# Kernel tuning notes

Hardware: AMD Instinct MI355X
Metric: run time of the kernel (lower is better)

Reference implementation:

```python
import jax, jax.numpy as jnp
import numpy as np

B = 32768
DNA, IMG, FUSED, HEADS = 768, 512, 256, 4
HEAD_DIM = FUSED // HEADS
GENUS, SPECIES, MAXSP = 372, 1050, 23
RED, GEMB, SDH, DEC_HID = 128, 64, 64, 744


def setup_inputs() -> dict:
    key = jax.random.key(0)
    ks = iter(jax.random.split(key, 40))
    p = lambda *shape: jax.random.normal(next(ks), shape, jnp.float32) * 0.02
    z = lambda n: jnp.zeros((n,), jnp.float32)
    inp = {
        'dna_emb': jax.random.normal(next(ks), (B, DNA), jnp.float32),
        'img_emb': jax.random.normal(next(ks), (B, IMG), jnp.float32),
        # AttentionFusion params
        'W_dna': p(DNA, FUSED), 'b_dna': z(FUSED),
        'W_img': p(IMG, FUSED), 'b_img': z(FUSED),
        'W_qkv': p(FUSED, 3 * FUSED), 'b_qkv': z(3 * FUSED),
        'W_o': p(FUSED, FUSED), 'b_o': z(FUSED),
        'W_f1': p(FUSED, FUSED), 'b_f1': z(FUSED),
        'W_f2': p(FUSED, FUSED), 'b_f2': z(FUSED),
        # genus Decoder params
        'W_d1': p(FUSED, DEC_HID), 'b_d1': z(DEC_HID),
        'W_d2': p(DEC_HID, GENUS), 'b_d2': z(GENUS),
        # SpeciePredictor params
        'W_fp': p(FUSED, RED), 'b_fp': z(RED),
        'W_ge': p(GENUS, GEMB), 'b_ge': z(GEMB),
        'W_s1': p(RED + GEMB, SDH), 'b_s1': z(SDH),
        'W_s2': p(SDH, MAXSP), 'b_s2': z(MAXSP),
        # precomputed scatter->gather indices: species s -> (genus s%372, local s//372)
        'species_genus': jnp.arange(SPECIES, dtype=jnp.int32) % GENUS,
        'species_local': jnp.arange(SPECIES, dtype=jnp.int32) // GENUS,
    }
    return inp


def _forward(dna_emb, img_emb, W_dna, b_dna, W_img, b_img, W_qkv, b_qkv, W_o, b_o,
             W_f1, b_f1, W_f2, b_f2, W_d1, b_d1, W_d2, b_d2, W_fp, b_fp,
             W_ge, b_ge, W_s1, b_s1, W_s2, b_s2, species_genus, species_local):
    # --- AttentionFusion ---
    dna_proj = dna_emb @ W_dna + b_dna                     # [B, F]
    img_proj = img_emb @ W_img + b_img                     # [B, F]
    seq = jnp.stack([dna_proj, img_proj], axis=1)          # [B, 2, F]
    qkv = seq @ W_qkv + b_qkv                              # [B, 2, 3F]
    q, k, v = jnp.split(qkv, 3, axis=-1)
    q = q.reshape(B, 2, HEADS, HEAD_DIM)
    k = k.reshape(B, 2, HEADS, HEAD_DIM)
    v = v.reshape(B, 2, HEADS, HEAD_DIM)
    scale = 1.0 / np.sqrt(HEAD_DIM).astype(np.float32)
    scores = jnp.einsum('bqhd,bkhd->bhqk', q, k) * scale   # [B, H, 2, 2]
    attn = jax.nn.softmax(scores, axis=-1)
    ctx = jnp.einsum('bhqk,bkhd->bqhd', attn, v).reshape(B, 2, FUSED)
    attn_out = ctx @ W_o + b_o                             # [B, 2, F]
    fused = attn_out.mean(axis=1)                          # [B, F]
    fused = jax.nn.relu(fused @ W_f1 + b_f1) @ W_f2 + b_f2
    # --- genus Decoder (Linear -> Sigmoid -> Linear -> softmax) ---
    genus_logits = jax.nn.softmax(
        jax.nn.sigmoid(fused @ W_d1 + b_d1) @ W_d2 + b_d2, axis=1)  # [B, 372]
    # --- species head ---
    reduced_fused = fused @ W_fp + b_fp                    # [B, 128]
    genus_emb = genus_logits @ W_ge + b_ge                 # [B, 64]
    genus_fused = jnp.concatenate([genus_emb, reduced_fused], axis=1)  # [B, 192]
    local_logits = jax.nn.sigmoid(genus_fused @ W_s1 + b_s1) @ W_s2 + b_s2  # [B, 23]
    # --- _flatten_species_probs_batch, fused: result[:, s] = genus_logits[:, g(s)] * local_logits[:, l(s)]
    # (avoids materializing the [B, 372, 23] outer product)
    species_probs = genus_logits[:, species_genus] * local_logits[:, species_local]  # [B, 1050]
    return species_probs, local_logits, genus_logits, fused, reduced_fused


def reference(dna_emb, img_emb, W_dna, b_dna, W_img, b_img, W_qkv, b_qkv, W_o, b_o,
              W_f1, b_f1, W_f2, b_f2, W_d1, b_d1, W_d2, b_d2, W_fp, b_fp,
              W_ge, b_ge, W_s1, b_s1, W_s2, b_s2, species_genus, species_local):
    return _forward(dna_emb, img_emb, W_dna, b_dna, W_img, b_img, W_qkv, b_qkv,
                    W_o, b_o, W_f1, b_f1, W_f2, b_f2, W_d1, b_d1, W_d2, b_d2,
                    W_fp, b_fp, W_ge, b_ge, W_s1, b_s1, W_s2, b_s2,
                    species_genus, species_local)
```

## Files before the change

kernel.cpp:

```cpp
#include <hip/hip_runtime.h>
#include <hip/hip_bf16.h>

typedef __hip_bfloat16 bf16;
typedef __attribute__((ext_vector_type(8))) short short8_t;
typedef __attribute__((ext_vector_type(4))) float f32x4;

#define B_ROWS 32768

__device__ __forceinline__ float to_f(float x) { return x; }
__device__ __forceinline__ float to_f(bf16 x) { return __bfloat162float(x); }

__device__ __forceinline__ unsigned short f2bf(float f) {
    union { float f; unsigned int u; } c; c.f = f;
    unsigned int u = c.u;
    unsigned int rb = ((u >> 16) & 1u) + 0x7fffu;
    return (unsigned short)((u + rb) >> 16);
}

__device__ __forceinline__ void stage8(const bf16* __restrict__ src, bf16* dst) {
    *(uint4*)dst = *(const uint4*)src;
}
__device__ __forceinline__ void stage8(const float* __restrict__ src, bf16* dst) {
    const float4 a = *(const float4*)src;
    const float4 b = *(const float4*)(src + 4);
    union { uint4 u; unsigned short h[8]; } r;
    r.h[0] = f2bf(a.x); r.h[1] = f2bf(a.y); r.h[2] = f2bf(a.z); r.h[3] = f2bf(a.w);
    r.h[4] = f2bf(b.x); r.h[5] = f2bf(b.y); r.h[6] = f2bf(b.z); r.h[7] = f2bf(b.w);
    *(uint4*)dst = r.u;
}

template <typename TA, int ACT>
__global__ __launch_bounds__(256) void gemm_mfma(
    const TA* __restrict__ A, int lda,
    const bf16* __restrict__ Wt, int kpad,
    const float* __restrict__ bias,
    float* __restrict__ outf, int ldof,
    bf16* __restrict__ outb, int ldob,
    int M, int N, int nstore, int K)
{
    __shared__ __align__(16) bf16 As[128 * 64];
    __shared__ __align__(16) bf16 Bs[128 * 64];

    const int tid = threadIdx.x;
    const int lane = tid & 63;
    const int w = tid >> 6;
    const int wr = w >> 1, wc = w & 1;
    const int m0 = blockIdx.y * 128, n0 = blockIdx.x * 128;
    const int kq = lane >> 4, lr = lane & 15;

    f32x4 acc[4][4] = {};

    const int srow = tid >> 3;
    const int sch = tid & 7;
    const int sx = sch ^ (srow & 7);

    for (int k0 = 0; k0 < K; k0 += 64) {
#pragma unroll
        for (int p = 0; p < 4; ++p) {
            const int row = srow + p * 32;
            const int dst = row * 64 + (sx << 3);
            stage8(A + (size_t)(m0 + row) * lda + (k0 + sch * 8), &As[dst]);
            stage8(Wt + (size_t)(n0 + row) * kpad + (k0 + sch * 8), &Bs[dst]);
        }
        __syncthreads();
#pragma unroll
        for (int kk = 0; kk < 2; ++kk) {
            const int co = ((kk * 4 + kq) ^ (lr & 7)) << 3;
            short8_t am[4], wf[4];
#pragma unroll
            for (int i = 0; i < 4; ++i) {
                am[i] = *(const short8_t*)&As[(wr * 64 + i * 16 + lr) * 64 + co];
                wf[i] = *(const short8_t*)&Bs[(wc * 64 + i * 16 + lr) * 64 + co];
            }
#pragma unroll
            for (int i = 0; i < 4; ++i)
#pragma unroll
                for (int j = 0; j < 4; ++j)
                    acc[i][j] = __builtin_amdgcn_mfma_f32_16x16x32_bf16(
                        wf[j], am[i], acc[i][j], 0, 0, 0);
        }
        __syncthreads();
    }

#pragma unroll
    for (int mi = 0; mi < 4; ++mi) {
        const size_t m = m0 + wr * 64 + mi * 16 + lr;
#pragma unroll
        for (int ni = 0; ni < 4; ++ni) {
            const int nb = n0 + wc * 64 + ni * 16 + 4 * kq;
            if (nb >= nstore) continue;
            float vv[4];
#pragma unroll
            for (int r = 0; r < 4; ++r) {
                const int n = nb + r;
                float v = acc[mi][ni][r] + ((n < N) ? bias[n] : 0.f);
                if (ACT == 1) v = fmaxf(v, 0.f);
                if (ACT == 2) v = (n < N) ? 1.f / (1.f + __expf(-v)) : 0.f;
                vv[r] = v;
            }
            if (outf) {
                if (nb + 3 < N) {
                    float4 f4; f4.x = vv[0]; f4.y = vv[1]; f4.z = vv[2]; f4.w = vv[3];
                    *(float4*)&outf[m * ldof + nb] = f4;
                } else {
#pragma unroll
                    for (int r = 0; r < 4; ++r)
                        if (nb + r < N) outf[m * ldof + nb + r] = vv[r];
                }
            }
            if (outb) {
                if (nb + 3 < nstore) {
                    union { uint2 u; unsigned short h[4]; } pk;
                    pk.h[0] = f2bf(vv[0]); pk.h[1] = f2bf(vv[1]);
                    pk.h[2] = f2bf(vv[2]); pk.h[3] = f2bf(vv[3]);
                    *(uint2*)&outb[m * ldob + nb] = pk.u;
                } else {
#pragma unroll
                    for (int r = 0; r < 4; ++r)
                        if (nb + r < nstore)
                            ((unsigned short*)outb)[m * ldob + nb + r] = f2bf(vv[r]);
                }
            }
        }
    }
}

struct PrepackArgs {
    const float* src[12];
    unsigned long long off[12];
    int K[12], N[12], Kpad[12], Nr[12];
};

__global__ __launch_bounds__(256) void prepack_kernel(PrepackArgs a, bf16* wsbase)
{
    const int wI = blockIdx.y;
    const float* __restrict__ src = a.src[wI];
    bf16* dst = wsbase + a.off[wI];
    const int K = a.K[wI], N = a.N[wI], Kpad = a.Kpad[wI];
    const int total = a.Nr[wI] * Kpad;
    for (int e = blockIdx.x * 256 + threadIdx.x; e < total; e += gridDim.x * 256) {
        const int n = e / Kpad, k = e - n * Kpad;
        const float v = (n < N && k < K) ? src[(size_t)k * N + n] : 0.f;
        ((unsigned short*)dst)[e] = f2bf(v);
    }
}

__global__ __launch_bounds__(256) void attn_kernel(
    const bf16* __restrict__ qkv, bf16* __restrict__ ctxm)
{
    const int b = blockIdx.x;
    const int lane = threadIdx.x & 63;
    const bf16* base = qkv + (size_t)b * 1536;
    const int o = (threadIdx.x >> 6) * 64 + lane;

    float q0 = to_f(base[o]),       k0 = to_f(base[256 + o]),       v0 = to_f(base[512 + o]);
    float q1 = to_f(base[768 + o]), k1 = to_f(base[768 + 256 + o]), v1 = to_f(base[768 + 512 + o]);

    float s00 = q0 * k0, s01 = q0 * k1, s10 = q1 * k0, s11 = q1 * k1;
#pragma unroll
    for (int off = 32; off; off >>= 1) {
        s00 += __shfl_xor(s00, off);
        s01 += __shfl_xor(s01, off);
        s10 += __shfl_xor(s10, off);
        s11 += __shfl_xor(s11, off);
    }
    const float sc = 0.125f;
    s00 *= sc; s01 *= sc; s10 *= sc; s11 *= sc;

    float m0 = fmaxf(s00, s01);
    float e00 = __expf(s00 - m0), e01 = __expf(s01 - m0);
    float r0 = 1.f / (e00 + e01);
    float m1 = fmaxf(s10, s11);
    float e10 = __expf(s10 - m1), e11 = __expf(s11 - m1);
    float r1 = 1.f / (e10 + e11);

    float c0 = e00 * r0 * v0 + e01 * r0 * v1;
    float c1 = e10 * r1 * v0 + e11 * r1 * v1;
    ctxm[(size_t)b * 256 + o] = __float2bfloat16(0.5f * (c0 + c1));
}

__global__ __launch_bounds__(64) void softmax372_kernel(
    const bf16* __restrict__ in, float* __restrict__ outf, bf16* __restrict__ outb)
{
    const int b = blockIdx.x;
    const int lane = threadIdx.x;
    const bf16* row = in + (size_t)b * 372;

    float v[6];
    float mx = -1e30f;
#pragma unroll
    for (int i = 0; i < 6; ++i) {
        int idx = lane + i * 64;
        v[i] = (idx < 372) ? to_f(row[idx]) : -1e30f;
        mx = fmaxf(mx, v[i]);
    }
#pragma unroll
    for (int off = 32; off; off >>= 1) mx = fmaxf(mx, __shfl_xor(mx, off));

    float s = 0.f;
#pragma unroll
    for (int i = 0; i < 6; ++i) {
        int idx = lane + i * 64;
        if (idx < 372) { v[i] = __expf(v[i] - mx); s += v[i]; }
    }
#pragma unroll
    for (int off = 32; off; off >>= 1) s += __shfl_xor(s, off);
    float r = 1.f / s;

#pragma unroll
    for (int i = 0; i < 6; ++i) {
        int idx = lane + i * 64;
        if (idx < 372) {
            float p = v[i] * r;
            outf[(size_t)b * 372 + idx] = p;
            outb[(size_t)b * 384 + idx] = __float2bfloat16(p);
        } else if (idx < 384) {
            outb[(size_t)b * 384 + idx] = __float2bfloat16(0.f);
        }
    }
}

__global__ __launch_bounds__(256) void species_kernel(
    const float* __restrict__ g, const float* __restrict__ ll,
    const int* __restrict__ sg, const int* __restrict__ sl,
    float* __restrict__ out)
{
    const int s = blockIdx.x * 256 + threadIdx.x;
    const int b = blockIdx.y;
    if (s < 1050) {
        out[(size_t)b * 1050 + s] =
            g[(size_t)b * 372 + sg[s]] * ll[(size_t)b * 23 + sl[s]];
    }
}

extern "C" void kernel_launch(void* const* d_in, const int* in_sizes, int n_in,
                              void* d_out, int out_size, void* d_ws, size_t ws_size,
                              hipStream_t stream)
{
    const int B = B_ROWS;
    const float* dna   = (const float*)d_in[0];
    const float* img   = (const float*)d_in[1];
    const float* W_dna = (const float*)d_in[2];  const float* b_dna = (const float*)d_in[3];
    const float* W_img = (const float*)d_in[4];  const float* b_img = (const float*)d_in[5];
    const float* W_qkv = (const float*)d_in[6];  const float* b_qkv = (const float*)d_in[7];
    const float* W_o   = (const float*)d_in[8];  const float* b_o   = (const float*)d_in[9];
    const float* W_f1  = (const float*)d_in[10]; const float* b_f1  = (const float*)d_in[11];
    const float* W_f2  = (const float*)d_in[12]; const float* b_f2  = (const float*)d_in[13];
    const float* W_d1  = (const float*)d_in[14]; const float* b_d1  = (const float*)d_in[15];
    const float* W_d2  = (const float*)d_in[16]; const float* b_d2  = (const float*)d_in[17];
    const float* W_fp  = (const float*)d_in[18]; const float* b_fp  = (const float*)d_in[19];
    const float* W_ge  = (const float*)d_in[20]; const float* b_ge  = (const float*)d_in[21];
    const float* W_s1  = (const float*)d_in[22]; const float* b_s1  = (const float*)d_in[23];
    const float* W_s2  = (const float*)d_in[24]; const float* b_s2  = (const float*)d_in[25];
    const int*   sg    = (const int*)d_in[26];
    const int*   sl    = (const int*)d_in[27];

    bf16* ws = (bf16*)d_ws;

    static const int KK[12] = {768, 512, 256, 256, 256, 256, 256, 744, 256, 372, 192, 64};
    static const int NN[12] = {256, 256, 768, 256, 256, 256, 744, 372, 128,  64,  64, 23};
    const float* SRC[12] = {W_dna, W_img, W_qkv, W_o, W_f1, W_f2, W_d1, W_d2, W_fp, W_ge, W_s1, W_s2};
    PrepackArgs pa;
    size_t woff[12];
    size_t off = 0;
    for (int i = 0; i < 12; ++i) {
        pa.src[i] = SRC[i]; pa.K[i] = KK[i]; pa.N[i] = NN[i];
        pa.Kpad[i] = (KK[i] + 63) & ~63;
        pa.Nr[i]   = (NN[i] + 127) & ~127;
        pa.off[i] = off; woff[i] = off;
        off += (size_t)pa.Kpad[i] * pa.Nr[i];
    }
    const size_t AOFF = off;

    bf16* seq  = ws + AOFF;
    bf16* qkvc = ws + AOFF + (size_t)B * 512;
    bf16* ctxm = ws + AOFF + (size_t)B * 896;
    bf16* t1   = ws + AOFF;
    bf16* t2   = ws + AOFF + (size_t)B * 256;
    bf16* fbuf = ws + AOFF;
    bf16* h1   = ws + AOFF + (size_t)B * 256;
    bf16* g    = ws + AOFF + (size_t)B * 1024;
    bf16* gbf  = ws + AOFF + (size_t)B * 256;
    bf16* gf   = ws + AOFF + (size_t)B * 640;
    bf16* sh   = ws + AOFF + (size_t)B * 832;

    float* out       = (float*)d_out;
    float* o_species = out;
    float* o_local   = out + (size_t)B * 1050;
    float* o_genus   = out + (size_t)B * 1073;
    float* o_fused   = out + (size_t)B * 1445;
    float* o_red     = out + (size_t)B * 1701;

    prepack_kernel<<<dim3(32, 12), 256, 0, stream>>>(pa, ws);

#define NOF (float*)nullptr, 0
#define NOB (bf16*)nullptr, 0

    gemm_mfma<float, 0><<<dim3(2, 256), 256, 0, stream>>>(
        dna, 768, ws + woff[0], 768, b_dna, NOF, seq, 512, B, 256, 256, 768);
    gemm_mfma<float, 0><<<dim3(2, 256), 256, 0, stream>>>(
        img, 512, ws + woff[1], 512, b_img, NOF, seq + 256, 512, B, 256, 256, 512);
    for (int c = 0; c < 4; ++c) {
        gemm_mfma<bf16, 0><<<dim3(6, 128), 256, 0, stream>>>(
            seq + (size_t)c * (B / 2) * 256, 256, ws + woff[2], 256, b_qkv,
            NOF, qkvc, 768, B / 2, 768, 768, 256);
        attn_kernel<<<B / 4, 256, 0, stream>>>(qkvc, ctxm + (size_t)c * (B / 4) * 256);
    }
    gemm_mfma<bf16, 0><<<dim3(2, 256), 256, 0, stream>>>(
        ctxm, 256, ws + woff[3], 256, b_o, NOF, t1, 256, B, 256, 256, 256);
    gemm_mfma<bf16, 1><<<dim3(2, 256), 256, 0, stream>>>(
        t1, 256, ws + woff[4], 256, b_f1, NOF, t2, 256, B, 256, 256, 256);
    gemm_mfma<bf16, 0><<<dim3(2, 256), 256, 0, stream>>>(
        t2, 256, ws + woff[5], 256, b_f2, o_fused, 256, fbuf, 256, B, 256, 256, 256);
    gemm_mfma<bf16, 2><<<dim3(6, 256), 256, 0, stream>>>(
        fbuf, 256, ws + woff[6], 256, b_d1, NOF, h1, 768, B, 744, 768, 256);
    gemm_mfma<bf16, 0><<<dim3(3, 256), 256, 0, stream>>>(
        h1, 768, ws + woff[7], 768, b_d2, NOF, g, 372, B, 372, 372, 768);
    softmax372_kernel<<<B, 64, 0, stream>>>(g, o_genus, gbf);
    gemm_mfma<bf16, 0><<<dim3(1, 256), 256, 0, stream>>>(
        gbf, 384, ws + woff[9], 384, b_ge, NOF, gf, 192, B, 64, 64, 384);
    gemm_mfma<bf16, 0><<<dim3(1, 256), 256, 0, stream>>>(
        fbuf, 256, ws + woff[8], 256, b_fp, o_red, 128, gf + 64, 192, B, 128, 128, 256);
    gemm_mfma<bf16, 2><<<dim3(1, 256), 256, 0, stream>>>(
        gf, 192, ws + woff[10], 192, b_s1, NOF, sh, 64, B, 64, 64, 192);
    gemm_mfma<bf16, 0><<<dim3(1, 256), 256, 0, stream>>>(
        sh, 64, ws + woff[11], 64, b_s2, o_local, 23, NOB, B, 23, 23, 64);
    species_kernel<<<dim3(5, B), 256, 0, stream>>>(o_genus, o_local, sg, sl, o_species);
#undef NOF
#undef NOB
}
```

Before: 854.8 us.

## Fuse fusion MLP chain, use direct-to-LDS loads, widen GEMM tiles, unchunk QKV

Several changes land together. A new mlp3 kernel chains the W_o, W_f1 and W_f2 GEMMs per 128-row tile, keeping the intermediates in shared memory instead of writing them to global memory. GEMM staging of bf16 data now goes through global_load_lds straight into LDS, and most GEMMs use a 256-wide N tile with 512 threads. The QKV GEMM and attention run once over the whole batch instead of in four chunks, and the weight prepack uses a shared-memory transpose. This cuts global memory traffic and launch count, at the cost of much more LDS per block (the mlp3 kernel uses about 112KB), which may limit occupancy.

```diff
diff --git a/kernel.cpp b/kernel.cpp
--- a/kernel.cpp
+++ b/kernel.cpp
@@ -17,10 +17,13 @@
     return (unsigned short)((u + rb) >> 16);
 }
 
-__device__ __forceinline__ void stage8(const bf16* __restrict__ src, bf16* dst) {
-    *(uint4*)dst = *(const uint4*)src;
-}
-__device__ __forceinline__ void stage8(const float* __restrict__ src, bf16* dst) {
+__device__ __forceinline__ void glds16(const void* g, void* s) {
+    __builtin_amdgcn_global_load_lds(
+        (const __attribute__((address_space(1))) unsigned int*)g,
+        (__attribute__((address_space(3))) unsigned int*)s, 16, 0, 0);
+}
+
+__device__ __forceinline__ void stage8f(const float* __restrict__ src, bf16* dst) {
     const float4 a = *(const float4*)src;
     const float4 b = *(const float4*)(src + 4);
     union { uint4 u; unsigned short h[8]; } r;
@@ -29,8 +32,8 @@
     *(uint4*)dst = r.u;
 }
 
-template <typename TA, int ACT>
-__global__ __launch_bounds__(256) void gemm_mfma(
+template <typename TA, int BN, int ACT>
+__global__ __launch_bounds__(BN * 2) void gemm_mfma(
     const TA* __restrict__ A, int lda,
     const bf16* __restrict__ Wt, int kpad,
     const float* __restrict__ bias,
@@ -38,29 +41,42 @@
     bf16* __restrict__ outb, int ldob,
     int M, int N, int nstore, int K)
 {
+    constexpr int NT = BN * 2;
+    constexpr int WC = BN / 64;
     __shared__ __align__(16) bf16 As[128 * 64];
-    __shared__ __align__(16) bf16 Bs[128 * 64];
+    __shared__ __align__(16) bf16 Bs[BN * 64];
 
     const int tid = threadIdx.x;
     const int lane = tid & 63;
     const int w = tid >> 6;
-    const int wr = w >> 1, wc = w & 1;
-    const int m0 = blockIdx.y * 128, n0 = blockIdx.x * 128;
+    const int wr = w / WC, wc = w % WC;
+    const int m0 = blockIdx.y * 128, n0 = blockIdx.x * BN;
     const int kq = lane >> 4, lr = lane & 15;
 
     f32x4 acc[4][4] = {};
 
-    const int srow = tid >> 3;
-    const int sch = tid & 7;
-    const int sx = sch ^ (srow & 7);
-
     for (int k0 = 0; k0 < K; k0 += 64) {
-#pragma unroll
-        for (int p = 0; p < 4; ++p) {
-            const int row = srow + p * 32;
-            const int dst = row * 64 + (sx << 3);
-            stage8(A + (size_t)(m0 + row) * lda + (k0 + sch * 8), &As[dst]);
-            stage8(Wt + (size_t)(n0 + row) * kpad + (k0 + sch * 8), &Bs[dst]);
+        if constexpr (sizeof(TA) == 2) {
+#pragma unroll
+            for (int j = 0; j < 1024 / NT; ++j) {
+                const int c = tid + j * NT;
+                const int row = c >> 3, sx = (c & 7) ^ (row & 7);
+                glds16(A + (size_t)(m0 + row) * lda + k0 + sx * 8, &As[c * 8]);
+            }
+        } else {
+#pragma unroll
+            for (int j = 0; j < 1024 / NT; ++j) {
+                const int c = tid + j * NT;
+                const int row = c >> 3, sx = (c & 7) ^ (row & 7);
+                stage8f(A + (size_t)(m0 + row) * lda + k0 + (c & 7) * 8,
+                        &As[row * 64 + sx * 8]);
+            }
+        }
+#pragma unroll
+        for (int j = 0; j < BN * 8 / NT; ++j) {
+            const int c = tid + j * NT;
+            const int row = c >> 3, sx = (c & 7) ^ (row & 7);
+            glds16(Wt + (size_t)(n0 + row) * kpad + k0 + sx * 8, &Bs[c * 8]);
         }
         __syncthreads();
 #pragma unroll
@@ -125,6 +141,128 @@
     }
 }
 
+#define MLP3_STAGE_W(WP)                                                       \
+    _Pragma("unroll")                                                          \
+    for (int j = 0; j < 4; ++j) {                                              \
+        const int c = tid + j * 512;                                           \
+        const int row = c >> 3, sx = (c & 7) ^ (row & 7);                      \
+        glds16(WP + (size_t)row * 256 + ks * 64 + sx * 8, &Wb[c * 8]);         \
+    }
+
+#define MLP3_COMPUTE(ASRC)                                                     \
+    _Pragma("unroll")                                                          \
+    for (int kk = 0; kk < 2; ++kk) {                                           \
+        const int co = ((kk * 4 + kq) ^ (lr & 7)) << 3;                        \
+        short8_t am[4], wf[4];                                                 \
+        _Pragma("unroll")                                                      \
+        for (int i = 0; i < 4; ++i) {                                          \
+            am[i] = *(const short8_t*)&(ASRC)[(wr * 64 + i * 16 + lr) * 64 + co]; \
+            wf[i] = *(const short8_t*)&Wb[(wc * 64 + i * 16 + lr) * 64 + co];  \
+        }                                                                      \
+        _Pragma("unroll")                                                      \
+        for (int i = 0; i < 4; ++i)                                            \
+            _Pragma("unroll")                                                  \
+            for (int j2 = 0; j2 < 4; ++j2)                                     \
+                acc[i][j2] = __builtin_amdgcn_mfma_f32_16x16x32_bf16(          \
+                    wf[j2], am[i], acc[i][j2], 0, 0, 0);                       \
+    }
+
+#define MLP3_STORE_T(BIASP, RELU)                                              \
+    _Pragma("unroll")                                                          \
+    for (int mi = 0; mi < 4; ++mi) {                                           \
+        const int m = wr * 64 + mi * 16 + lr;                                  \
+        _Pragma("unroll")                                                      \
+        for (int ni = 0; ni < 4; ++ni) {                                       \
+            const int nb = wc * 64 + ni * 16 + 4 * kq;                         \
+            union { unsigned long long u; unsigned short h[4]; } pk;           \
+            _Pragma("unroll")                                                  \
+            for (int r = 0; r < 4; ++r) {                                      \
+                float v = acc[mi][ni][r] + BIASP[nb + r];                      \
+                if (RELU) v = fmaxf(v, 0.f);                                   \
+                pk.h[r] = f2bf(v);                                             \
+            }                                                                  \
+            *(unsigned long long*)&T[nb >> 6]                                  \
+                [m * 64 + ((((nb & 63) >> 3) ^ (m & 7)) << 3) + (nb & 7)] = pk.u; \
+        }                                                                      \
+    }
+
+#define ZERO_ACC                                                               \
+    _Pragma("unroll")                                                          \
+    for (int i = 0; i < 4; ++i)                                                \
+        _Pragma("unroll")                                                      \
+        for (int j2 = 0; j2 < 4; ++j2) acc[i][j2] = f32x4{0.f, 0.f, 0.f, 0.f};
+
+__global__ __launch_bounds__(512) void mlp3_kernel(
+    const bf16* __restrict__ ctxm,
+    const bf16* __restrict__ Wo, const float* __restrict__ b_o,
+    const bf16* __restrict__ Wf1, const float* __restrict__ b_f1,
+    const bf16* __restrict__ Wf2, const float* __restrict__ b_f2,
+    float* __restrict__ o_fused, bf16* __restrict__ fbuf)
+{
+    __shared__ __align__(16) bf16 Ab[128 * 64];
+    __shared__ __align__(16) bf16 Wb[256 * 64];
+    __shared__ __align__(16) bf16 T[4][128 * 64];
+
+    const int tid = threadIdx.x, lane = tid & 63, w = tid >> 6;
+    const int wr = w >> 2, wc = w & 3;
+    const int m0 = blockIdx.x * 128;
+    const int kq = lane >> 4, lr = lane & 15;
+
+    f32x4 acc[4][4];
+    ZERO_ACC
+
+    for (int ks = 0; ks < 4; ++ks) {
+#pragma unroll
+        for (int j = 0; j < 2; ++j) {
+            const int c = tid + j * 512;
+            const int row = c >> 3, sx = (c & 7) ^ (row & 7);
+            glds16(ctxm + (size_t)(m0 + row) * 256 + ks * 64 + sx * 8, &Ab[c * 8]);
+        }
+        MLP3_STAGE_W(Wo)
+        __syncthreads();
+        MLP3_COMPUTE(Ab)
+        __syncthreads();
+    }
+    MLP3_STORE_T(b_o, false)
+    __syncthreads();
+
+    ZERO_ACC
+    for (int ks = 0; ks < 4; ++ks) {
+        MLP3_STAGE_W(Wf1)
+        __syncthreads();
+        MLP3_COMPUTE(T[ks])
+        __syncthreads();
+    }
+    MLP3_STORE_T(b_f1, true)
+    __syncthreads();
+
+    ZERO_ACC
+    for (int ks = 0; ks < 4; ++ks) {
+        MLP3_STAGE_W(Wf2)
+        __syncthreads();
+        MLP3_COMPUTE(T[ks])
+        __syncthreads();
+    }
+#pragma unroll
+    for (int mi = 0; mi < 4; ++mi) {
+        const size_t m = m0 + wr * 64 + mi * 16 + lr;
+#pragma unroll
+        for (int ni = 0; ni < 4; ++ni) {
+            const int nb = wc * 64 + ni * 16 + 4 * kq;
+            float vv[4];
+            union { unsigned long long u; unsigned short h[4]; } pk;
+#pragma unroll
+            for (int r = 0; r < 4; ++r) {
+                vv[r] = acc[mi][ni][r] + b_f2[nb + r];
+                pk.h[r] = f2bf(vv[r]);
+            }
+            float4 f4; f4.x = vv[0]; f4.y = vv[1]; f4.z = vv[2]; f4.w = vv[3];
+            *(float4*)&o_fused[m * 256 + nb] = f4;
+            *(unsigned long long*)&fbuf[m * 256 + nb] = pk.u;
+        }
+    }
+}
+
 struct PrepackArgs {
     const float* src[12];
     unsigned long long off[12];
@@ -137,11 +275,25 @@
     const float* __restrict__ src = a.src[wI];
     bf16* dst = wsbase + a.off[wI];
     const int K = a.K[wI], N = a.N[wI], Kpad = a.Kpad[wI];
-    const int total = a.Nr[wI] * Kpad;
-    for (int e = blockIdx.x * 256 + threadIdx.x; e < total; e += gridDim.x * 256) {
-        const int n = e / Kpad, k = e - n * Kpad;
-        const float v = (n < N && k < K) ? src[(size_t)k * N + n] : 0.f;
-        ((unsigned short*)dst)[e] = f2bf(v);
+    const int tilesK = Kpad >> 6, tilesN = a.Nr[wI] >> 6;
+    __shared__ float tile[64][65];
+
+    for (int t = blockIdx.x; t < tilesK * tilesN; t += gridDim.x) {
+        const int k0 = (t % tilesK) << 6, n0 = (t / tilesK) << 6;
+        const int cc = threadIdx.x & 63, rr = threadIdx.x >> 6;
+#pragma unroll
+        for (int i = 0; i < 16; ++i) {
+            const int k = k0 + rr + i * 4, n = n0 + cc;
+            tile[rr + i * 4][cc] = (k < K && n < N) ? src[(size_t)k * N + n] : 0.f;
+        }
+        __syncthreads();
+#pragma unroll
+        for (int i = 0; i < 16; ++i) {
+            const int nl = rr + i * 4;
+            ((unsigned short*)dst)[(size_t)(n0 + nl) * Kpad + k0 + cc] =
+                f2bf(tile[cc][nl]);
+        }
+        __syncthreads();
     }
 }
 
@@ -266,23 +418,21 @@
     for (int i = 0; i < 12; ++i) {
         pa.src[i] = SRC[i]; pa.K[i] = KK[i]; pa.N[i] = NN[i];
         pa.Kpad[i] = (KK[i] + 63) & ~63;
-        pa.Nr[i]   = (NN[i] + 127) & ~127;
+        pa.Nr[i]   = (NN[i] + 255) & ~255;
         pa.off[i] = off; woff[i] = off;
         off += (size_t)pa.Kpad[i] * pa.Nr[i];
     }
     const size_t AOFF = off;
 
     bf16* seq  = ws + AOFF;
-    bf16* qkvc = ws + AOFF + (size_t)B * 512;
-    bf16* ctxm = ws + AOFF + (size_t)B * 896;
-    bf16* t1   = ws + AOFF;
-    bf16* t2   = ws + AOFF + (size_t)B * 256;
-    bf16* fbuf = ws + AOFF;
-    bf16* h1   = ws + AOFF + (size_t)B * 256;
-    bf16* g    = ws + AOFF + (size_t)B * 1024;
-    bf16* gbf  = ws + AOFF + (size_t)B * 256;
-    bf16* gf   = ws + AOFF + (size_t)B * 640;
-    bf16* sh   = ws + AOFF + (size_t)B * 832;
+    bf16* qkvf = ws + AOFF + (size_t)B * 512;
+    bf16* ctxm = ws + AOFF;
+    bf16* fbuf = ws + AOFF + (size_t)B * 256;
+    bf16* h1   = ws + AOFF + (size_t)B * 512;
+    bf16* g    = ws + AOFF + (size_t)B * 1280;
+    bf16* gbf  = ws + AOFF + (size_t)B * 512;
+    bf16* gf   = ws + AOFF + (size_t)B * 896;
+    bf16* sh   = ws + AOFF + (size_t)B * 1088;
 
     float* out       = (float*)d_out;
     float* o_species = out;
@@ -291,39 +441,33 @@
     float* o_fused   = out + (size_t)B * 1445;
     float* o_red     = out + (size_t)B * 1701;
 
-    prepack_kernel<<<dim3(32, 12), 256, 0, stream>>>(pa, ws);
+    prepack_kernel<<<dim3(64, 12), 256, 0, stream>>>(pa, ws);
 
 #define NOF (float*)nullptr, 0
 #define NOB (bf16*)nullptr, 0
 
-    gemm_mfma<float, 0><<<dim3(2, 256), 256, 0, stream>>>(
+    gemm_mfma<float, 256, 0><<<dim3(1, 256), 512, 0, stream>>>(
         dna, 768, ws + woff[0], 768, b_dna, NOF, seq, 512, B, 256, 256, 768);
-    gemm_mfma<float, 0><<<dim3(2, 256), 256, 0, stream>>>(
+    gemm_mfma<float, 256, 0><<<dim3(1, 256), 512, 0, stream>>>(
         img, 512, ws + woff[1], 512, b_img, NOF, seq + 256, 512, B, 256, 256, 512);
-    for (int c = 0; c < 4; ++c) {
-        gemm_mfma<bf16, 0><<<dim3(6, 128), 256, 0, stream>>>(
-            seq + (size_t)c * (B / 2) * 256, 256, ws + woff[2], 256, b_qkv,
-            NOF, qkvc, 768, B / 2, 768, 768, 256);
-        attn_kernel<<<B / 4, 256, 0, stream>>>(qkvc, ctxm + (size_t)c * (B / 4) * 256);
-    }
-    gemm_mfma<bf16, 0><<<dim3(2, 256), 256, 0, stream>>>(
-        ctxm, 256, ws + woff[3], 256, b_o, NOF, t1, 256, B, 256, 256, 256);
-    gemm_mfma<bf16, 1><<<dim3(2, 256), 256, 0, stream>>>(
-        t1, 256, ws + woff[4], 256, b_f1, NOF, t2, 256, B, 256, 256, 256);
-    gemm_mfma<bf16, 0><<<dim3(2, 256), 256, 0, stream>>>(
-        t2, 256, ws + woff[5], 256, b_f2, o_fused, 256, fbuf, 256, B, 256, 256, 256);
-    gemm_mfma<bf16, 2><<<dim3(6, 256), 256, 0, stream>>>(
+    gemm_mfma<bf16, 256, 0><<<dim3(3, 512), 512, 0, stream>>>(
+        seq, 256, ws + woff[2], 256, b_qkv, NOF, qkvf, 768, 2 * B, 768, 768, 256);
+    attn_kernel<<<B, 256, 0, stream>>>(qkvf, ctxm);
+    mlp3_kernel<<<256, 512, 0, stream>>>(
+        ctxm, ws + woff[3], b_o, ws + woff[4], b_f1, ws + woff[5], b_f2,
+        o_fused, fbuf);
+    gemm_mfma<bf16, 256, 2><<<dim3(3, 256), 512, 0, stream>>>(
         fbuf, 256, ws + woff[6], 256, b_d1, NOF, h1, 768, B, 744, 768, 256);
-    gemm_mfma<bf16, 0><<<dim3(3, 256), 256, 0, stream>>>(
+    gemm_mfma<bf16, 256, 0><<<dim3(2, 256), 512, 0, stream>>>(
         h1, 768, ws + woff[7], 768, b_d2, NOF, g, 372, B, 372, 372, 768);
     softmax372_kernel<<<B, 64, 0, stream>>>(g, o_genus, gbf);
-    gemm_mfma<bf16, 0><<<dim3(1, 256), 256, 0, stream>>>(
+    gemm_mfma<bf16, 128, 0><<<dim3(1, 256), 256, 0, stream>>>(
         gbf, 384, ws + woff[9], 384, b_ge, NOF, gf, 192, B, 64, 64, 384);
-    gemm_mfma<bf16, 0><<<dim3(1, 256), 256, 0, stream>>>(
+    gemm_mfma<bf16, 128, 0><<<dim3(1, 256), 256, 0, stream>>>(
         fbuf, 256, ws + woff[8], 256, b_fp, o_red, 128, gf + 64, 192, B, 128, 128, 256);
-    gemm_mfma<bf16, 2><<<dim3(1, 256), 256, 0, stream>>>(
+    gemm_mfma<bf16, 128, 2><<<dim3(1, 256), 256, 0, stream>>>(
         gf, 192, ws + woff[10], 192, b_s1, NOF, sh, 64, B, 64, 64, 192);
-    gemm_mfma<bf16, 0><<<dim3(1, 256), 256, 0, stream>>>(
+    gemm_mfma<bf16, 128, 0><<<dim3(1, 256), 256, 0, stream>>>(
         sh, 64, ws + woff[11], 64, b_s2, o_local, 23, NOB, B, 23, 23, 64);
     species_kernel<<<dim3(5, B), 256, 0, stream>>>(o_genus, o_local, sg, sl, o_species);
 #undef NOF
```

New measurement: 804.1 us. 5.9% less time.
